# Optimization experiments

Measured on AMD Instinct MI355X. Metric: run time of the kernel, lower is better.

## Reference

```python
import jax, jax.numpy as jnp
import numpy as np

NUM_HEADS = 10
LN_EPS = 1e-5

def setup_inputs() -> dict:
    key = jax.random.key(0)
    ks = jax.random.split(key, 8)
    B, H, N, D, Dt = 256, 200, 64, 640, 256
    s = 0.02
    return {
        'clicked_news': jax.random.normal(ks[0], (B, H, D), jnp.float32),
        'clicked_topics': jax.random.normal(ks[1], (B, H, Dt), jnp.float32),
        'cand_topics': jax.random.normal(ks[2], (B, N, Dt), jnp.float32),
        'Wq': jax.random.normal(ks[3], (D, Dt), jnp.float32) * s,
        'bq': jnp.zeros((D,), jnp.float32),
        'Wk': jax.random.normal(ks[4], (D, Dt), jnp.float32) * s,
        'bk': jnp.zeros((D,), jnp.float32),
        'Wv': jax.random.normal(ks[5], (D, D), jnp.float32) * s,
        'bv': jnp.zeros((D,), jnp.float32),
        'Wg': jax.random.normal(ks[6], (D, D), jnp.float32) * s,
        'bg': jnp.zeros((D,), jnp.float32),
        'ln_gamma': jnp.ones((D,), jnp.float32),
        'ln_beta': jnp.zeros((D,), jnp.float32),
    }

def reference(clicked_news, clicked_topics, cand_topics, Wq, bq, Wk, bk, Wv, bv, Wg, bg, ln_gamma, ln_beta):
    B, H, D = clicked_news.shape
    N = cand_topics.shape[1]
    nh = NUM_HEADS
    hd = D // nh
    scale = jnp.sqrt(jnp.asarray(D, clicked_news.dtype))

    Qf = cand_topics @ Wq.T + bq            # [B, N, D]
    Kf = clicked_topics @ Wk.T + bk         # [B, H, D]
    # V projection feeds `weighted`, which is dead code w.r.t. outputs; omitted.

    Q = Qf.reshape(B, N, nh, hd)
    K = Kf.reshape(B, H, nh, hd)
    scores = jnp.einsum('bnhd,bmhd->bhnm', Q, K) / scale   # [B, nh, N, H]
    attn = jax.nn.softmax(scores, axis=-1)                 # dropout is identity in eval

    # query weighting: softmax over candidates of ||Q||
    query_weights = jax.nn.softmax(jnp.linalg.norm(Qf, axis=-1), axis=1)   # [B, N]
    agg = (attn.sum(axis=1) * query_weights[:, :, None]).sum(axis=1)       # [B, H]
    attn_weights_agg = jax.nn.softmax(agg, axis=-1)                        # [B, H]

    weighted_clicked = attn_weights_agg[:, :, None] * clicked_news         # [B, H, D]
    gate = jax.nn.sigmoid(weighted_clicked @ Wg.T + bg)
    out = gate * weighted_clicked + (1.0 - gate) * clicked_news

    mu = out.mean(axis=-1, keepdims=True)
    var = out.var(axis=-1, keepdims=True)
    out = (out - mu) / jnp.sqrt(var + LN_EPS) * ln_gamma + ln_beta
    return out, attn_weights_agg
```

## Files before the change

kernel.cpp:

```cpp
#include <hip/hip_runtime.h>
#include <math.h>

#define B_  256
#define H_  200
#define N_  64
#define D_  640
#define DT_ 256
#define NH_ 10
#define HD_ 64
#define MT_ 13
#define MH_ 25600

typedef __attribute__((ext_vector_type(8))) short bf16x8;
typedef __attribute__((ext_vector_type(4))) float f32x4;

__device__ __forceinline__ float wave_reduce_sum(float v) {
    #pragma unroll
    for (int m = 32; m > 0; m >>= 1) v += __shfl_xor(v, m);
    return v;
}
__device__ __forceinline__ float wave_reduce_max(float v) {
    #pragma unroll
    for (int m = 32; m > 0; m >>= 1) v = fmaxf(v, __shfl_xor(v, m));
    return v;
}
__device__ __forceinline__ float red16_sum(float v) {
    #pragma unroll
    for (int m = 1; m < 16; m <<= 1) v += __shfl_xor(v, m);
    return v;
}
__device__ __forceinline__ float red16_max(float v) {
    #pragma unroll
    for (int m = 1; m < 16; m <<= 1) v = fmaxf(v, __shfl_xor(v, m));
    return v;
}
__device__ __forceinline__ short f2bf(float x) {
    unsigned u = __float_as_uint(x);
    unsigned r = (u + 0x7fffu + ((u >> 16) & 1u)) >> 16;
    return (short)r;
}
__device__ __forceinline__ float bf2f(short s) {
    return __uint_as_float(((unsigned)(unsigned short)s) << 16);
}

__device__ __forceinline__ void gload_lds16(const void* g, void* lds) {
    __builtin_amdgcn_global_load_lds(
        (const __attribute__((address_space(1))) void*)g,
        (__attribute__((address_space(3))) void*)lds, 16, 0, 0);
}

__global__ __launch_bounds__(256) void convert3(
    const float* __restrict__ s0, short* __restrict__ d0, int n0,
    const float* __restrict__ s1, short* __restrict__ d1, int n1,
    const float* __restrict__ s2, short* __restrict__ d2, int n2)
{
    const int total = n0 + n1 + n2;
    for (int i = blockIdx.x * 256 + threadIdx.x; i < total; i += gridDim.x * 256) {
        if (i < n0)            d0[i] = f2bf(s0[i]);
        else if (i < n0 + n1)  d1[i - n0] = f2bf(s1[i - n0]);
        else                   d2[i - n0 - n1] = f2bf(s2[i - n0 - n1]);
    }
}

__device__ __forceinline__ void gemm_tile(
    const float* __restrict__ A, int lda,
    const short* __restrict__ Wb, int ldb,
    const float* __restrict__ bias,
    short* __restrict__ Y, int nkc, float* __restrict__ qss,
    int row0, int col0,
    float* A_f, short* B_lds, int t)
{
    const int lane = t & 63, w = t >> 6;
    const int wm = w >> 1, wn = w & 1;
    const int r16 = lane & 15, g = lane >> 4;

    f32x4 acc[4][2];
    #pragma unroll
    for (int ct = 0; ct < 4; ++ct) {
        acc[ct][0] = (f32x4){0.f,0.f,0.f,0.f};
        acc[ct][1] = (f32x4){0.f,0.f,0.f,0.f};
    }

    for (int k = 0; k < nkc; ++k) {
        const int k0 = k * 64;
        #pragma unroll
        for (int j = 0; j < 4; ++j) {
            const int u = t + j * 256;
            const int row = u >> 4, jj = u & 15;
            gload_lds16(A + (long)(row0 + row) * lda + k0 + ((jj ^ (row & 7)) << 2),
                        (char*)A_f + u * 16);
        }
        #pragma unroll
        for (int j = 0; j < 4; ++j) {
            const int u = t + j * 256;
            const int col = u >> 3, jj = u & 7;
            gload_lds16(Wb + (long)(col0 + col) * ldb + k0 + ((jj ^ (col & 7)) << 3),
                        (char*)B_lds + u * 16);
        }
        __syncthreads();

        #pragma unroll
        for (int kk = 0; kk < 2; ++kk) {
            bf16x8 a[2];
            #pragma unroll
            for (int rt = 0; rt < 2; ++rt) {
                const int row = wm * 32 + rt * 16 + r16;
                const int s = kk * 8 + g * 2;
                float4 f0 = *(const float4*)(A_f + row * 64 + ((s ^ (row & 7)) << 2));
                float4 f1 = *(const float4*)(A_f + row * 64 + (((s + 1) ^ (row & 7)) << 2));
                bf16x8 av;
                av[0] = f2bf(f0.x); av[1] = f2bf(f0.y); av[2] = f2bf(f0.z); av[3] = f2bf(f0.w);
                av[4] = f2bf(f1.x); av[5] = f2bf(f1.y); av[6] = f2bf(f1.z); av[7] = f2bf(f1.w);
                a[rt] = av;
            }
            #pragma unroll
            for (int ct = 0; ct < 4; ++ct) {
                const int col = wn * 64 + ct * 16 + r16;
                const int sb = kk * 4 + g;
                bf16x8 b = *(const bf16x8*)(B_lds + col * 64 + ((sb ^ (col & 7)) << 3));
                acc[ct][0] = __builtin_amdgcn_mfma_f32_16x16x32_bf16(a[0], b, acc[ct][0], 0, 0, 0);
                acc[ct][1] = __builtin_amdgcn_mfma_f32_16x16x32_bf16(a[1], b, acc[ct][1], 0, 0, 0);
            }
        }
        __syncthreads();
    }

    float ps[2][4];
    #pragma unroll
    for (int rt = 0; rt < 2; ++rt)
        #pragma unroll
        for (int i = 0; i < 4; ++i) ps[rt][i] = 0.f;

    #pragma unroll
    for (int ct = 0; ct < 4; ++ct) {
        const int col = col0 + wn * 64 + ct * 16 + r16;
        const float bv = bias ? bias[col] : 0.f;
        #pragma unroll
        for (int rt = 0; rt < 2; ++rt)
            #pragma unroll
            for (int i = 0; i < 4; ++i) {
                const short ob = f2bf(acc[ct][rt][i] + bv);
                Y[(long)(row0 + wm * 32 + rt * 16 + g * 4 + i) * D_ + col] = ob;
                if (qss) { const float of = bf2f(ob); ps[rt][i] += of * of; }
            }
    }
    if (qss) {
        const int strip = col0 >> 7;
        #pragma unroll
        for (int rt = 0; rt < 2; ++rt)
            #pragma unroll
            for (int i = 0; i < 4; ++i) {
                const float s = red16_sum(ps[rt][i]);
                if (r16 == 0) {
                    const int row = row0 + wm * 32 + rt * 16 + g * 4 + i;
                    qss[(long)row * 10 + strip * 2 + wn] = s;
                }
            }
    }
}

__global__ __launch_bounds__(256, 5) void gemm_bt(
    const float* __restrict__ A, int lda,
    const short* __restrict__ Wb, int ldb,
    const float* __restrict__ bias,
    short* __restrict__ Y, int nkc)
{
    __shared__ float A_f[64 * 64];
    __shared__ short B_lds[128 * 64];
    const int lb = (blockIdx.x & 7) * ((int)gridDim.x >> 3) + (blockIdx.x >> 3);
    gemm_tile(A, lda, Wb, ldb, bias, Y, nkc, nullptr,
              (lb / 5) * 64, (lb % 5) * 128, A_f, B_lds, threadIdx.x);
}

#define NQB 1280
#define NKB 4000
__global__ __launch_bounds__(256, 5) void proj2(
    const float* __restrict__ Aq, const short* __restrict__ Wqb,
    const float* __restrict__ bq, short* __restrict__ Yq, float* __restrict__ qss,
    const float* __restrict__ Ak, const short* __restrict__ Wkb,
    const float* __restrict__ bk, short* __restrict__ Yk)
{
    __shared__ float A_f[64 * 64];
    __shared__ short B_lds[128 * 64];
    const int lb = (blockIdx.x & 7) * ((int)gridDim.x >> 3) + (blockIdx.x >> 3);
    if (lb < NQB) {
        gemm_tile(Aq, DT_, Wqb, DT_, bq, Yq, 4, qss,
                  (lb / 5) * 64, (lb % 5) * 128, A_f, B_lds, threadIdx.x);
    } else {
        const int kb = lb - NQB;
        gemm_tile(Ak, DT_, Wkb, DT_, bk, Yk, 4, nullptr,
                  (kb / 5) * 64, (kb % 5) * 128, A_f, B_lds, threadIdx.x);
    }
}

__global__ __launch_bounds__(512, 2) void attn2(
    const short* __restrict__ Qb, const short* __restrict__ Kb,
    const float* __restrict__ qss,
    float* __restrict__ aw, float* __restrict__ out_tail)
{
    __shared__ short K_l[2][2][208 * 64];
    __shared__ float qw_l[N_];
    __shared__ float aggp[8][MT_ * 16];
    __shared__ float red2[2];
    const int t = threadIdx.x;
    const int lane = t & 63, w = t >> 6;
    const int wm = w & 3, hh = w >> 2;
    const int r16 = lane & 15, g = lane >> 4;
    const int b = blockIdx.x;
    const int tt = t & 255;
    const int half = t >> 8;

    auto STAGE_K = [&](int bi, int hi) {
        const int h = half * 5 + hi;
        #pragma unroll
        for (int j = 0; j < 7; ++j) {
            const int u = tt + j * 256;
            if (u < 208 * 8) {
                const int row = u >> 3, jg = u & 7;
                gload_lds16(Kb + ((long)(b * H_) + row) * D_ + h * HD_ +
                                ((jg ^ (row & 7)) << 3),
                            (char*)K_l[half][bi] + u * 16);
            }
        }
    };

    STAGE_K(0, 0);

    if (w == 0) {
        const float* qp = qss + ((long)(b * N_ + lane)) * 10;
        float ss = 0.f;
        #pragma unroll
        for (int j = 0; j < 10; ++j) ss += qp[j];
        float v = sqrtf(ss);
        float mx = wave_reduce_max(v);
        float e = __expf(v - mx);
        float s = wave_reduce_sum(e);
        qw_l[lane] = e / s;
    }
    __syncthreads();

    float qwr[4];
    #pragma unroll
    for (int i = 0; i < 4; ++i) qwr[i] = qw_l[wm * 16 + g * 4 + i];

    const float inv_scale = 0.0395284707521047f;
    float aggl[MT_];
    #pragma unroll
    for (int mt = 0; mt < MT_; ++mt) aggl[mt] = 0.f;

    for (int hi = 0; hi < 5; ++hi) {
        const int h = hh * 5 + hi;
        if (hi + 1 < 5) STAGE_K((hi + 1) & 1, hi + 1);

        const short* kl = K_l[hh][hi & 1];
        const short* qbase = Qb + ((long)(b * N_ + wm * 16 + r16)) * D_ + h * HD_ + g * 8;
        bf16x8 a0 = *(const bf16x8*)(qbase);
        bf16x8 a1 = *(const bf16x8*)(qbase + 32);
        bf16x8 kb0[MT_], kb1[MT_];
        #pragma unroll
        for (int mt = 0; mt < MT_; ++mt) {
            const int row = mt * 16 + r16;
            const int s0 = g ^ (row & 7);
            const int s1 = (g + 4) ^ (row & 7);
            kb0[mt] = *(const bf16x8*)(kl + row * 64 + s0 * 8);
            kb1[mt] = *(const bf16x8*)(kl + row * 64 + s1 * 8);
        }
        f32x4 acc[MT_];
        #pragma unroll
        for (int mt = 0; mt < MT_; ++mt) {
            f32x4 z = {0.f,0.f,0.f,0.f};
            z = __builtin_amdgcn_mfma_f32_16x16x32_bf16(a0, kb0[mt], z, 0, 0, 0);
            z = __builtin_amdgcn_mfma_f32_16x16x32_bf16(a1, kb1[mt], z, 0, 0, 0);
            acc[mt] = z;
        }
        const bool tailok = (r16 < 8);
        float mx[4] = {-INFINITY, -INFINITY, -INFINITY, -INFINITY};
        #pragma unroll
        for (int mt = 0; mt < MT_; ++mt) {
            const bool valid = (mt < 12) || tailok;
            #pragma unroll
            for (int i = 0; i < 4; ++i)
                if (valid) mx[i] = fmaxf(mx[i], acc[mt][i]);
        }
        #pragma unroll
        for (int i = 0; i < 4; ++i) mx[i] = red16_max(mx[i]);
        float sum[4] = {0.f, 0.f, 0.f, 0.f};
        #pragma unroll
        for (int mt = 0; mt < MT_; ++mt) {
            const bool valid = (mt < 12) || tailok;
            #pragma unroll
            for (int i = 0; i < 4; ++i) {
                float e = valid ? __expf((acc[mt][i] - mx[i]) * inv_scale) : 0.f;
                acc[mt][i] = e;
                sum[i] += e;
            }
        }
        float fct[4];
        #pragma unroll
        for (int i = 0; i < 4; ++i) fct[i] = qwr[i] / red16_sum(sum[i]);
        #pragma unroll
        for (int mt = 0; mt < MT_; ++mt)
            aggl[mt] += acc[mt][0] * fct[0] + acc[mt][1] * fct[1]
                      + acc[mt][2] * fct[2] + acc[mt][3] * fct[3];

        __syncthreads();
    }

    #pragma unroll
    for (int mt = 0; mt < MT_; ++mt) {
        aggl[mt] += __shfl_xor(aggl[mt], 16);
        aggl[mt] += __shfl_xor(aggl[mt], 32);
    }
    if (g == 0) {
        #pragma unroll
        for (int mt = 0; mt < MT_; ++mt) aggp[w][mt * 16 + r16] = aggl[mt];
    }
    __syncthreads();
    if (t < MT_ * 16) {
        float v = 0.f;
        #pragma unroll
        for (int j = 0; j < 8; ++j) v += aggp[j][t];
        aggp[0][t] = v;
    }
    __syncthreads();
    if (w == 0) {
        float v0 = aggp[0][lane], v1 = aggp[0][lane + 64], v2 = aggp[0][lane + 128];
        const bool has3 = lane < (H_ - 192);
        float v3 = has3 ? aggp[0][lane + 192] : -INFINITY;
        float mx = wave_reduce_max(fmaxf(fmaxf(v0, v1), fmaxf(v2, v3)));
        float s = __expf(v0 - mx) + __expf(v1 - mx) + __expf(v2 - mx)
                + (has3 ? __expf(v3 - mx) : 0.f);
        s = wave_reduce_sum(s);
        if (lane == 0) { red2[0] = mx; red2[1] = s; }
    }
    __syncthreads();
    if (t < H_) {
        float v = __expf(aggp[0][t] - red2[0]) / red2[1];
        aw[b * H_ + t] = v;
        out_tail[b * H_ + t] = v;
    }
}

__global__ __launch_bounds__(256) void blendln(
    const float* __restrict__ cl, const short* __restrict__ Z,
    const float* __restrict__ aw, const float* __restrict__ bg,
    const float* __restrict__ gamma, const float* __restrict__ beta,
    float* __restrict__ out)
{
    const int t = threadIdx.x;
    const int lane = t & 63, w = t >> 6;
    const int row = blockIdx.x * 4 + w;
    const float awr = aw[row];
    const long base = (long)row * D_;

    float o[10];
    float s = 0.f, sq = 0.f;
    #pragma unroll
    for (int i = 0; i < 10; ++i) {
        const int col = lane + 64 * i;
        const float y = bf2f(Z[base + col]);
        const float c = cl[base + col];
        const float z = awr * y + bg[col];
        const float gt = 1.f / (1.f + __expf(-z));
        const float ov = c * (1.f + gt * (awr - 1.f));
        o[i] = ov; s += ov; sq += ov * ov;
    }
    s  = wave_reduce_sum(s);
    sq = wave_reduce_sum(sq);
    const float mu  = s * (1.f / D_);
    const float var = sq * (1.f / D_) - mu * mu;
    const float ri  = 1.0f / sqrtf(var + 1e-5f);
    #pragma unroll
    for (int i = 0; i < 10; ++i) {
        const int col = lane + 64 * i;
        out[base + col] = (o[i] - mu) * ri * gamma[col] + beta[col];
    }
}

extern "C" void kernel_launch(void* const* d_in, const int* in_sizes, int n_in,
                              void* d_out, int out_size, void* d_ws, size_t ws_size,
                              hipStream_t stream) {
    const float* clicked_news   = (const float*)d_in[0];
    const float* clicked_topics = (const float*)d_in[1];
    const float* cand_topics    = (const float*)d_in[2];
    const float* Wq = (const float*)d_in[3];
    const float* bq = (const float*)d_in[4];
    const float* Wk = (const float*)d_in[5];
    const float* bk = (const float*)d_in[6];
    const float* Wg = (const float*)d_in[9];
    const float* bg = (const float*)d_in[10];
    const float* ln_gamma = (const float*)d_in[11];
    const float* ln_beta  = (const float*)d_in[12];

    float* out = (float*)d_out;
    float* ws  = (float*)d_ws;

    float* aw   = ws;
    short* Wq_b = (short*)(aw + (long)B_ * H_);
    short* Wk_b = Wq_b + (long)D_ * DT_;
    short* Wg_b = Wk_b + (long)D_ * DT_;
    float* qss  = (float*)(Wg_b + (long)D_ * D_);
    short* Qb   = (short*)(qss + (long)B_ * N_ * 10);
    short* Z    = Qb;
    short* Kb = (short*)d_out;
    float* out_tail = out + (long)B_ * H_ * D_;

    convert3<<<1440, 256, 0, stream>>>(Wq, Wq_b, D_ * DT_,
                                       Wk, Wk_b, D_ * DT_,
                                       Wg, Wg_b, D_ * D_);

    proj2<<<NQB + NKB, 256, 0, stream>>>(cand_topics, Wq_b, bq, Qb, qss,
                                         clicked_topics, Wk_b, bk, Kb);
    attn2<<<B_, 512, 0, stream>>>(Qb, Kb, qss, aw, out_tail);

    for (int h = 0; h < 2; ++h) {
        const long off = (long)h * MH_;
        gemm_bt<<<2000, 256, 0, stream>>>(clicked_news + off * D_, D_,
                                          Wg_b, D_, nullptr, Z, 10);
        blendln<<<MH_ / 4, 256, 0, stream>>>(
            clicked_news + off * D_, Z, aw + off, bg, ln_gamma, ln_beta,
            out + off * D_);
    }
}
```

Before: 264.2 us.

## Pre-convert topic activations to bf16 and use async LDS loads in projection GEMM

The converter kernel now also casts cand_topics and clicked_topics to bf16 in workspace, and the Q/K projection uses a new bf16-A tile routine. That routine streams both operands into LDS with global_load_lds in two 128-wide K steps, replacing the in-loop fp32-to-bf16 conversion. This is meant to cut per-tile conversion work and halve A-tile LDS traffic. In exchange it adds an extra global write/read pass over about 16M activation elements and lowers the occupancy hint from 5 to 3 blocks for the larger LDS footprint.

```diff
diff --git a/kernel.cpp b/kernel.cpp
--- a/kernel.cpp
+++ b/kernel.cpp
@@ -49,16 +49,21 @@
         (__attribute__((address_space(3))) void*)lds, 16, 0, 0);
 }
 
-__global__ __launch_bounds__(256) void convert3(
+__global__ __launch_bounds__(256) void convert5(
     const float* __restrict__ s0, short* __restrict__ d0, int n0,
     const float* __restrict__ s1, short* __restrict__ d1, int n1,
-    const float* __restrict__ s2, short* __restrict__ d2, int n2)
-{
-    const int total = n0 + n1 + n2;
+    const float* __restrict__ s2, short* __restrict__ d2, int n2,
+    const float* __restrict__ s3, short* __restrict__ d3, int n3,
+    const float* __restrict__ s4, short* __restrict__ d4, int n4)
+{
+    const int e01 = n0 + n1, e02 = n0 + n1 + n2, e03 = e02 + n3;
+    const int total = e03 + n4;
     for (int i = blockIdx.x * 256 + threadIdx.x; i < total; i += gridDim.x * 256) {
-        if (i < n0)            d0[i] = f2bf(s0[i]);
-        else if (i < n0 + n1)  d1[i - n0] = f2bf(s1[i - n0]);
-        else                   d2[i - n0 - n1] = f2bf(s2[i - n0 - n1]);
+        if (i < n0)        d0[i] = f2bf(s0[i]);
+        else if (i < e01)  d1[i - n0] = f2bf(s1[i - n0]);
+        else if (i < e02)  d2[i - e01] = f2bf(s2[i - e01]);
+        else if (i < e03)  d3[i - e02] = f2bf(s3[i - e02]);
+        else               d4[i - e03] = f2bf(s4[i - e03]);
     }
 }
 
@@ -66,7 +71,7 @@
     const float* __restrict__ A, int lda,
     const short* __restrict__ Wb, int ldb,
     const float* __restrict__ bias,
-    short* __restrict__ Y, int nkc, float* __restrict__ qss,
+    short* __restrict__ Y, int nkc,
     int row0, int col0,
     float* A_f, short* B_lds, int t)
 {
@@ -125,6 +130,91 @@
         __syncthreads();
     }
 
+    #pragma unroll
+    for (int ct = 0; ct < 4; ++ct) {
+        const int col = col0 + wn * 64 + ct * 16 + r16;
+        const float bv = bias ? bias[col] : 0.f;
+        #pragma unroll
+        for (int rt = 0; rt < 2; ++rt)
+            #pragma unroll
+            for (int i = 0; i < 4; ++i)
+                Y[(long)(row0 + wm * 32 + rt * 16 + g * 4 + i) * D_ + col] =
+                    f2bf(acc[ct][rt][i] + bv);
+    }
+}
+
+__global__ __launch_bounds__(256, 5) void gemm_bt(
+    const float* __restrict__ A, int lda,
+    const short* __restrict__ Wb, int ldb,
+    const float* __restrict__ bias,
+    short* __restrict__ Y, int nkc)
+{
+    __shared__ float A_f[64 * 64];
+    __shared__ short B_lds[128 * 64];
+    const int lb = (blockIdx.x & 7) * ((int)gridDim.x >> 3) + (blockIdx.x >> 3);
+    gemm_tile(A, lda, Wb, ldb, bias, Y, nkc,
+              (lb / 5) * 64, (lb % 5) * 128, A_f, B_lds, threadIdx.x);
+}
+
+__device__ __forceinline__ void gemm_tile_bb(
+    const short* __restrict__ Ab,
+    const short* __restrict__ Wb,
+    const float* __restrict__ bias,
+    short* __restrict__ Y, float* __restrict__ qss,
+    int row0, int col0,
+    short* A_l, short* B_l, int t)
+{
+    const int lane = t & 63, w = t >> 6;
+    const int wm = w >> 1, wn = w & 1;
+    const int r16 = lane & 15, g = lane >> 4;
+
+    f32x4 acc[4][2];
+    #pragma unroll
+    for (int ct = 0; ct < 4; ++ct) {
+        acc[ct][0] = (f32x4){0.f,0.f,0.f,0.f};
+        acc[ct][1] = (f32x4){0.f,0.f,0.f,0.f};
+    }
+
+    #pragma unroll
+    for (int k = 0; k < 2; ++k) {
+        const int k0 = k * 128;
+        #pragma unroll
+        for (int j = 0; j < 4; ++j) {
+            const int u = t + j * 256;
+            const int row = u >> 4, jj = u & 15;
+            gload_lds16(Ab + (long)(row0 + row) * DT_ + k0 + ((jj ^ (row & 15)) << 3),
+                        (char*)A_l + u * 16);
+        }
+        #pragma unroll
+        for (int j = 0; j < 8; ++j) {
+            const int u = t + j * 256;
+            const int col = u >> 4, jj = u & 15;
+            gload_lds16(Wb + (long)(col0 + col) * DT_ + k0 + ((jj ^ (col & 15)) << 3),
+                        (char*)B_l + u * 16);
+        }
+        __syncthreads();
+
+        #pragma unroll
+        for (int kk = 0; kk < 4; ++kk) {
+            bf16x8 a[2];
+            #pragma unroll
+            for (int rt = 0; rt < 2; ++rt) {
+                const int row = wm * 32 + rt * 16 + r16;
+                const int s = kk * 4 + g;
+                a[rt] = *(const bf16x8*)(A_l + (row * 16 + (s ^ (row & 15))) * 8);
+            }
+            #pragma unroll
+            for (int ct = 0; ct < 4; ++ct) {
+                const int col = wn * 64 + ct * 16 + r16;
+                const int sb = kk * 4 + g;
+                bf16x8 b = *(const bf16x8*)(B_l + (col * 16 + (sb ^ (col & 15))) * 8);
+                acc[ct][0] = __builtin_amdgcn_mfma_f32_16x16x32_bf16(a[0], b, acc[ct][0], 0, 0, 0);
+                acc[ct][1] = __builtin_amdgcn_mfma_f32_16x16x32_bf16(a[1], b, acc[ct][1], 0, 0, 0);
+            }
+        }
+        __syncthreads();
+    }
+
     float ps[2][4];
     #pragma unroll
     for (int rt = 0; rt < 2; ++rt)
@@ -159,37 +249,24 @@
     }
 }
 
-__global__ __launch_bounds__(256, 5) void gemm_bt(
-    const float* __restrict__ A, int lda,
-    const short* __restrict__ Wb, int ldb,
-    const float* __restrict__ bias,
-    short* __restrict__ Y, int nkc)
-{
-    __shared__ float A_f[64 * 64];
-    __shared__ short B_lds[128 * 64];
-    const int lb = (blockIdx.x & 7) * ((int)gridDim.x >> 3) + (blockIdx.x >> 3);
-    gemm_tile(A, lda, Wb, ldb, bias, Y, nkc, nullptr,
-              (lb / 5) * 64, (lb % 5) * 128, A_f, B_lds, threadIdx.x);
-}
-
 #define NQB 1280
 #define NKB 4000
-__global__ __launch_bounds__(256, 5) void proj2(
-    const float* __restrict__ Aq, const short* __restrict__ Wqb,
+__global__ __launch_bounds__(256, 3) void proj2(
+    const short* __restrict__ Atq, const short* __restrict__ Wqb,
     const float* __restrict__ bq, short* __restrict__ Yq, float* __restrict__ qss,
-    const float* __restrict__ Ak, const short* __restrict__ Wkb,
+    const short* __restrict__ Atk, const short* __restrict__ Wkb,
     const float* __restrict__ bk, short* __restrict__ Yk)
 {
-    __shared__ float A_f[64 * 64];
-    __shared__ short B_lds[128 * 64];
+    __shared__ short A_l[64 * 128];
+    __shared__ short B_l[128 * 128];
     const int lb = (blockIdx.x & 7) * ((int)gridDim.x >> 3) + (blockIdx.x >> 3);
     if (lb < NQB) {
-        gemm_tile(Aq, DT_, Wqb, DT_, bq, Yq, 4, qss,
-                  (lb / 5) * 64, (lb % 5) * 128, A_f, B_lds, threadIdx.x);
+        gemm_tile_bb(Atq, Wqb, bq, Yq, qss,
+                     (lb / 5) * 64, (lb % 5) * 128, A_l, B_l, threadIdx.x);
     } else {
         const int kb = lb - NQB;
-        gemm_tile(Ak, DT_, Wkb, DT_, bk, Yk, 4, nullptr,
-                  (kb / 5) * 64, (kb % 5) * 128, A_f, B_lds, threadIdx.x);
+        gemm_tile_bb(Atk, Wkb, bk, Yk, nullptr,
+                     (kb / 5) * 64, (kb % 5) * 128, A_l, B_l, threadIdx.x);
     }
 }
 
@@ -400,17 +477,22 @@
     short* Wk_b = Wq_b + (long)D_ * DT_;
     short* Wg_b = Wk_b + (long)D_ * DT_;
     float* qss  = (float*)(Wg_b + (long)D_ * D_);
-    short* Qb   = (short*)(qss + (long)B_ * N_ * 10);
+    short* Atq  = (short*)(qss + (long)B_ * N_ * 10);
+    short* Qb   = Atq + (long)B_ * N_ * DT_;
+    short* Atk  = Qb + (long)B_ * N_ * D_;
     short* Z    = Qb;
     short* Kb = (short*)d_out;
     float* out_tail = out + (long)B_ * H_ * D_;
 
-    convert3<<<1440, 256, 0, stream>>>(Wq, Wq_b, D_ * DT_,
-                                       Wk, Wk_b, D_ * DT_,
-                                       Wg, Wg_b, D_ * D_);
-
-    proj2<<<NQB + NKB, 256, 0, stream>>>(cand_topics, Wq_b, bq, Qb, qss,
-                                         clicked_topics, Wk_b, bk, Kb);
+    convert5<<<2048, 256, 0, stream>>>(
+        Wq, Wq_b, D_ * DT_,
+        Wk, Wk_b, D_ * DT_,
+        Wg, Wg_b, D_ * D_,
+        cand_topics, Atq, B_ * N_ * DT_,
+        clicked_topics, Atk, B_ * H_ * DT_);
+
+    proj2<<<NQB + NKB, 256, 0, stream>>>(Atq, Wq_b, bq, Qb, qss,
+                                         Atk, Wk_b, bk, Kb);
     attn2<<<B_, 512, 0, stream>>>(Qb, Kb, qss, aw, out_tail);
 
     for (int h = 0; h < 2; ++h) {
```

Result: slower. 272.7 us (+3.2%).
